# Kernel optimization log

Hardware: AMD Instinct MI355X
Metric: run time of the kernel (lower is better)

## Reference

```python
import jax, jax.numpy as jnp
import numpy as np

BLOCK_SIZE = 32       # MXFP block size (OCP microscaling spec)
E2M1_MAX = 6.0        # max magnitude representable in FP4 E2M1
E2M1_EMAX = 2.0       # exponent of max binade (4..6)


def quantize_mxfp4(t):
    """Fake-quantize t to MXFP4 (E2M1 elements, E8M0 shared scale) along last dim.

    Matches MXFP_F.extract_mxfp_components + dequant: per block of 32 values a
    power-of-two shared scale 2^(floor(log2(amax)) - emax_elem), elements
    rounded to nearest E2M1 value {0, +-0.5, 1, 1.5, 2, 3, 4, 6}.
    """
    shp = t.shape
    tb = t.reshape(shp[:-1] + (shp[-1] // BLOCK_SIZE, BLOCK_SIZE))
    amax = jnp.max(jnp.abs(tb), axis=-1, keepdims=True)
    safe_amax = jnp.where(amax > 0, amax, 1.0)
    shared_exp = jnp.floor(jnp.log2(safe_amax)) - E2M1_EMAX  # E8M0 exponent
    scale = jnp.exp2(shared_exp)
    v = tb / scale
    av = jnp.abs(v)
    # E2M1 grid spacing: 0.5 in [0,2), 1 in [2,4), 2 in [4,6]
    e = jnp.clip(jnp.floor(jnp.log2(jnp.maximum(av, 2.0 ** -10))), 0.0, E2M1_EMAX)
    step = jnp.exp2(e - 1.0)  # one mantissa bit
    q = jnp.clip(jnp.round(av / step) * step, 0.0, E2M1_MAX) * jnp.sign(v)
    return (q * scale).reshape(shp)


def setup_inputs() -> dict:
    key = jax.random.key(0)
    kx, kw, kb = jax.random.split(key, 3)
    B, S, K, N = 2, 4096, 4096, 4096
    x = jax.random.normal(kx, (B, S, K), dtype=jnp.float32)
    weight = jax.random.normal(kw, (N, K), dtype=jnp.float32) * 0.02
    bias = jax.random.normal(kb, (N,), dtype=jnp.float32) * 0.02
    return {"x": x, "weight": weight, "bias": bias}


def reference(x, weight, bias):
    # layer_type 'XqWqB': quantize activations (block along in_features) and
    # weights (block_dim=1 == in_features); bias stays full precision.
    xq = quantize_mxfp4(x)                 # [B, S, K]
    wq = quantize_mxfp4(weight)            # [N, K]
    out = jnp.einsum("bsk,nk->bsn", xq, wq) + bias
    return out
```

## Files before the change

kernel.cpp:

```cpp
#include <hip/hip_runtime.h>
#include <hip/hip_bf16.h>

typedef __attribute__((ext_vector_type(4))) int i32x4;
typedef __attribute__((ext_vector_type(8))) int i32x8;
typedef __attribute__((ext_vector_type(16))) float f32x16;

#define GLOBAL_CPTR(x) ((__attribute__((address_space(1))) const void*)(x))
#define LDS_PTR(x)     ((__attribute__((address_space(3))) void*)(x))

__global__ __launch_bounds__(256) void mxfp4_quant_pack_kernel(
    const float* __restrict__ xin, unsigned char* __restrict__ xq,
    unsigned char* __restrict__ xsc, const float* __restrict__ win,
    unsigned char* __restrict__ wq, unsigned char* __restrict__ wsc,
    int kshift, int gx) {
  const int KC = 1 << (kshift - 5);
  const int CQ = KC >> 2;
  const int bid0 = blockIdx.x;
  const float* in;
  unsigned char* outq;
  unsigned char* outsc;
  int bid;
  if (bid0 < gx) { in = xin; outq = xq; outsc = xsc; bid = bid0; }
  else           { in = win; outq = wq; outsc = wsc; bid = bid0 - gx; }

  const int cq  = bid & (CQ - 1);
  const int R   = (bid >> (kshift - 7)) << 6;
  const int t   = threadIdx.x;

  __shared__ float sf[64 * 132];

  const float* base = in + ((size_t)R << kshift) + (cq << 7);
#pragma unroll
  for (int i = 0; i < 8; ++i) {
    const int g   = i * 256 + t;
    const int row = g >> 5;
    const int c4  = g & 31;
    float4 v = *reinterpret_cast<const float4*>(
        base + ((size_t)row << kshift) + (c4 << 2));
    *reinterpret_cast<float4*>(sf + row * 132 + (c4 << 2)) = v;
  }
  __syncthreads();

  const int rl = (t & 3) + ((t >> 4) << 2);
  const int kc = (t >> 2) & 3;
  const float* src = sf + rl * 132 + (kc << 5);
  float v[32];
#pragma unroll
  for (int i = 0; i < 8; ++i)
    *reinterpret_cast<float4*>(v + 4 * i) =
        *reinterpret_cast<const float4*>(src + 4 * i);

  float am = 0.f;
#pragma unroll
  for (int j = 0; j < 32; ++j) am = fmaxf(am, fabsf(v[j]));

  const float safe = am > 0.f ? am : 1.f;
  const int se = ilogbf(safe) - 2;
  const float inv = ldexpf(1.f, -se);

  unsigned int packs[4] = {0, 0, 0, 0};
#pragma unroll
  for (int j = 0; j < 32; ++j) {
    const float val = v[j] * inv;
    const float av = fabsf(val);
    const float avc = fmaxf(av, 9.765625e-4f);
    int ee = (int)((__float_as_uint(avc) >> 23) & 0xFF) - 127;
    ee = ee < 0 ? 0 : (ee > 2 ? 2 : ee);
    const float istep = __uint_as_float((unsigned)(128 - ee) << 23);
    const int m = (int)rintf(av * istep);
    unsigned int c = (unsigned)(m + (ee << 1));
    c = c > 7u ? 7u : c;
    c |= (__float_as_uint(val) >> 28) & 8u;
    packs[j >> 3] |= c << (4 * (j & 7));
  }

  const int row = R + rl;
  const size_t chunk = (size_t)(row >> 8) * KC + (cq << 2) + kc;
  *reinterpret_cast<uint4*>(outq + chunk * 4096 + (size_t)(row & 255) * 16) =
      make_uint4(packs[0], packs[1], packs[2], packs[3]);
  outsc[chunk * 256 + (row & 31) * 8 + ((row >> 5) & 7)] =
      (unsigned char)(se + 127);
}

#define BM 256
#define BN 256
#define NTHR 512
#define BUFS 18432

__global__ __launch_bounds__(NTHR, 2) void mxfp_gemm_kernel(
    const unsigned char* __restrict__ Aq, const unsigned char* __restrict__ Asc,
    const unsigned char* __restrict__ Bq, const unsigned char* __restrict__ Bsc,
    const float* __restrict__ bias, float* __restrict__ C,
    int M, int N, int K) {
  __shared__ unsigned char lds[2 * BUFS];

  const int tid = threadIdx.x;
  const int l   = tid & 63;
  const int wid = tid >> 6;
  const int wm  = wid >> 2;
  const int wn  = wid & 3;

  const int nwg = gridDim.x;
  const int bid = blockIdx.x;
  const int swz = (bid & 7) * (nwg >> 3) + (bid >> 3);
  const int nbn = N / BN;
  const int bm  = swz / nbn;
  const int bn  = swz % nbn;

  const int KC = K >> 5;

  const unsigned char* bLane = Bq + (((size_t)bn * KC) << 12) +
                               ((size_t)(l >> 5) << 12) + (wn << 10) +
                               ((l & 31) << 4);

  f32x16 acc[4][2] = {};

#define STAGE(BUFO, KT)                                                        \
  do {                                                                         \
    const int cl = wid & 3;                                                    \
    const int rg2 = (wid >> 2) << 1;                                           \
    const size_t abase = ((size_t)bm * KC + (size_t)(KT) * 4 + cl) * 4096;     \
    _Pragma("unroll") for (int i = 0; i < 2; ++i) {                            \
      __builtin_amdgcn_global_load_lds(                                        \
          GLOBAL_CPTR(Aq + abase + (rg2 + i) * 1024 + (l << 4)),               \
          LDS_PTR(lds + (BUFO) + cl * 4096 + (rg2 + i) * 1024), 16, 0, 0);     \
    }                                                                          \
    if (wid < 4) {                                                             \
      __builtin_amdgcn_global_load_lds(                                        \
          GLOBAL_CPTR(Asc + ((size_t)bm * KC + (size_t)(KT) * 4 + wid) * 256   \
                      + (l << 2)),                                             \
          LDS_PTR(lds + (BUFO) + 16384 + wid * 256), 4, 0, 0);                 \
    } else {                                                                   \
      __builtin_amdgcn_global_load_lds(                                        \
          GLOBAL_CPTR(Bsc + ((size_t)bn * KC + (size_t)(KT) * 4 + (wid - 4))   \
                      * 256 + (l << 2)),                                       \
          LDS_PTR(lds + (BUFO) + 17408 + (wid - 4) * 256), 4, 0, 0);           \
    }                                                                          \
  } while (0)

#define MFMA1(MB, NB, AV, BV)                                                  \
  acc[MB][NB] = __builtin_amdgcn_mfma_scale_f32_32x32x64_f8f6f4(               \
      a8[MB], b8[NB], acc[MB][NB], 4, 4, MB, AV, NB, BV)

#define KTILE(BUFO, KT)                                                        \
  do {                                                                         \
    const i32x4 z4 = {0, 0, 0, 0};                                             \
    const unsigned char* bt = bLane + ((size_t)(KT) << 14);                    \
    i32x4 braw[2][2];                                                          \
    _Pragma("unroll") for (int ks = 0; ks < 2; ++ks)                           \
      _Pragma("unroll") for (int nb = 0; nb < 2; ++nb)                         \
        braw[ks][nb] =                                                         \
            *(const i32x4*)(bt + (ks << 13) + (nb << 9));                      \
    _Pragma("unroll") for (int ks = 0; ks < 2; ++ks) {                         \
      const int cofs = (ks << 13) + ((l & 32) << 7);    \
      i32x8 a8[4], b8[2];                                                      \
      _Pragma("unroll") for (int mb = 0; mb < 4; ++mb)                         \
        a8[mb] = __builtin_shufflevector(                                      \
            *(const i32x4*)(lds + (BUFO) + cofs +                              \
                            (((wm << 7) + (mb << 5) + (l & 31)) << 4)),        \
            z4, 0, 1, 2, 3, 4, 5, 6, 7);                                       \
      _Pragma("unroll") for (int nb = 0; nb < 2; ++nb)                         \
        b8[nb] = __builtin_shufflevector(braw[ks][nb], z4,                     \
                                         0, 1, 2, 3, 4, 5, 6, 7);              \
      const int av = *(const int*)(lds + (BUFO) + 16384 + (cofs >> 4) +        \
                                   ((l & 31) << 3) + (wm << 2));               \
      const int bv = *(const ushort*)(lds + (BUFO) + 17408 + (cofs >> 4) +     \
                                      ((l & 31) << 3) + (wn << 1));            \
      MFMA1(0, 0, av, bv); MFMA1(0, 1, av, bv);                                \
      MFMA1(1, 0, av, bv); MFMA1(1, 1, av, bv);                                \
      MFMA1(2, 0, av, bv); MFMA1(2, 1, av, bv);                                \
      MFMA1(3, 0, av, bv); MFMA1(3, 1, av, bv);                                \
    }                                                                          \
  } while (0)

  STAGE(0, 0);
  asm volatile("s_waitcnt vmcnt(0)" ::: "memory");
  __builtin_amdgcn_s_barrier();
  asm volatile("" ::: "memory");

  const int NKT = K >> 7;
  for (int t = 0; t < NKT; ++t) {
    const int tn = (t + 1 < NKT) ? (t + 1) : t;
    const int bufC = (t & 1) ? BUFS : 0;
    const int bufN = (t & 1) ? 0 : BUFS;
    STAGE(bufN, tn);
    KTILE(bufC, t);
    asm volatile("s_waitcnt vmcnt(0)" ::: "memory");
    __builtin_amdgcn_s_barrier();
    asm volatile("" ::: "memory");
  }

  const int colb = bn * BN + wn * 64 + (l & 31);
  const int rowb = bm * BM + wm * 128 + ((l >> 5) << 2);
  const float bv0 = bias[colb];
  const float bv1 = bias[colb + 32];
#pragma unroll
  for (int mb = 0; mb < 4; ++mb) {
#pragma unroll
    for (int nb = 0; nb < 2; ++nb) {
      const float bv = nb ? bv1 : bv0;
      const int col = colb + nb * 32;
#pragma unroll
      for (int r = 0; r < 16; ++r) {
        const int row = rowb + mb * 32 + ((r >> 2) << 3) + (r & 3);
        C[(size_t)row * N + col] = acc[mb][nb][r] + bv;
      }
    }
  }
}

extern "C" void kernel_launch(void* const* d_in, const int* in_sizes, int n_in,
                              void* d_out, int out_size, void* d_ws, size_t ws_size,
                              hipStream_t stream) {
  const float* x    = (const float*)d_in[0];
  const float* w    = (const float*)d_in[1];
  const float* bias = (const float*)d_in[2];
  float* out = (float*)d_out;

  const int N = in_sizes[2];
  const int K = in_sizes[1] / N;
  const int M = (int)((long long)in_sizes[0] / K);
  const int kshift = __builtin_ctz(K);

  unsigned char* xq  = (unsigned char*)d_ws;
  unsigned char* wq  = xq + ((size_t)M * K >> 1);
  unsigned char* xsc = wq + ((size_t)N * K >> 1);
  unsigned char* wsc = xsc + ((size_t)M * K >> 5);

  const int CQ = (K >> 5) >> 2;
  const int gx = (M >> 6) * CQ;
  const int gw = (N >> 6) * CQ;

  mxfp4_quant_pack_kernel<<<dim3((unsigned)(gx + gw)), dim3(256), 0, stream>>>(
      x, xq, xsc, w, wq, wsc, kshift, gx);

  dim3 grid((M / BM) * (N / BN));
  mxfp_gemm_kernel<<<grid, dim3(NTHR), 0, stream>>>(xq, xsc, wq, wsc, bias, out,
                                                    M, N, K);
}
```

Before: 147.4 us.

## Shrink GEMM tile to 128x256 with 4 waves and stage B through LDS

The GEMM block tile drops from 256x256 with 8 waves to 128x256 with 4 waves. B tiles and scales are now staged through LDS with async global-to-LDS loads, where before each wave read them directly from global memory into registers. The A-side addressing and scale indexing are remapped onto the half-tile of the 256-row packed layout. The intent is more blocks and waves per CU (launch bounds raised to 3) and B fetches that overlap through the double buffer, at the cost of half the A reuse per block and more LDS per buffer.

```diff
diff --git a/kernel.cpp b/kernel.cpp
--- a/kernel.cpp
+++ b/kernel.cpp
@@ -82,12 +82,12 @@
       (unsigned char)(se + 127);
 }
 
-#define BM 256
+#define BM 128
 #define BN 256
-#define NTHR 512
-#define BUFS 18432
-
-__global__ __launch_bounds__(NTHR, 2) void mxfp_gemm_kernel(
+#define NTHR 256
+#define BUFS 26624
+
+__global__ __launch_bounds__(NTHR, 3) void mxfp_gemm_kernel(
     const unsigned char* __restrict__ Aq, const unsigned char* __restrict__ Asc,
     const unsigned char* __restrict__ Bq, const unsigned char* __restrict__ Bsc,
     const float* __restrict__ bias, float* __restrict__ C,
@@ -97,8 +97,7 @@
   const int tid = threadIdx.x;
   const int l   = tid & 63;
   const int wid = tid >> 6;
-  const int wm  = wid >> 2;
-  const int wn  = wid & 3;
+  const int wn  = wid;
 
   const int nwg = gridDim.x;
   const int bid = blockIdx.x;
@@ -109,62 +108,56 @@
 
   const int KC = K >> 5;
 
-  const unsigned char* bLane = Bq + (((size_t)bn * KC) << 12) +
-                               ((size_t)(l >> 5) << 12) + (wn << 10) +
-                               ((l & 31) << 4);
-
   f32x16 acc[4][2] = {};
 
 #define STAGE(BUFO, KT)                                                        \
   do {                                                                         \
-    const int cl = wid & 3;                                                    \
-    const int rg2 = (wid >> 2) << 1;                                           \
-    const size_t abase = ((size_t)bm * KC + (size_t)(KT) * 4 + cl) * 4096;     \
-    _Pragma("unroll") for (int i = 0; i < 2; ++i) {                            \
+    const size_t t4 = (size_t)(KT) * 4;                                        \
+    const size_t abase =                                                       \
+        ((size_t)(bm >> 1) * KC + t4 + wid) * 4096 + ((bm & 1) << 11);         \
+    _Pragma("unroll") for (int h = 0; h < 2; ++h)                              \
       __builtin_amdgcn_global_load_lds(                                        \
-          GLOBAL_CPTR(Aq + abase + (rg2 + i) * 1024 + (l << 4)),               \
-          LDS_PTR(lds + (BUFO) + cl * 4096 + (rg2 + i) * 1024), 16, 0, 0);     \
-    }                                                                          \
-    if (wid < 4) {                                                             \
+          GLOBAL_CPTR(Aq + abase + h * 1024 + (l << 4)),                       \
+          LDS_PTR(lds + (BUFO) + wid * 2048 + h * 1024), 16, 0, 0);            \
+    _Pragma("unroll") for (int c = 0; c < 4; ++c)                              \
       __builtin_amdgcn_global_load_lds(                                        \
-          GLOBAL_CPTR(Asc + ((size_t)bm * KC + (size_t)(KT) * 4 + wid) * 256   \
-                      + (l << 2)),                                             \
-          LDS_PTR(lds + (BUFO) + 16384 + wid * 256), 4, 0, 0);                 \
-    } else {                                                                   \
-      __builtin_amdgcn_global_load_lds(                                        \
-          GLOBAL_CPTR(Bsc + ((size_t)bn * KC + (size_t)(KT) * 4 + (wid - 4))   \
-                      * 256 + (l << 2)),                                       \
-          LDS_PTR(lds + (BUFO) + 17408 + (wid - 4) * 256), 4, 0, 0);           \
-    }                                                                          \
+          GLOBAL_CPTR(Bq + ((size_t)bn * KC + t4 + c) * 4096 + (wid << 10) +   \
+                      (l << 4)),                                               \
+          LDS_PTR(lds + (BUFO) + 8192 + c * 4096 + (wid << 10)), 16, 0, 0);    \
+    __builtin_amdgcn_global_load_lds(                                          \
+        GLOBAL_CPTR(Asc + ((size_t)(bm >> 1) * KC + t4 + wid) * 256 +          \
+                    (l << 2)),                                                 \
+        LDS_PTR(lds + (BUFO) + 24576 + (wid << 8)), 4, 0, 0);                  \
+    __builtin_amdgcn_global_load_lds(                                          \
+        GLOBAL_CPTR(Bsc + ((size_t)bn * KC + t4 + wid) * 256 + (l << 2)),      \
+        LDS_PTR(lds + (BUFO) + 25600 + (wid << 8)), 4, 0, 0);                  \
   } while (0)
 
 #define MFMA1(MB, NB, AV, BV)                                                  \
   acc[MB][NB] = __builtin_amdgcn_mfma_scale_f32_32x32x64_f8f6f4(               \
       a8[MB], b8[NB], acc[MB][NB], 4, 4, MB, AV, NB, BV)
 
-#define KTILE(BUFO, KT)                                                        \
+#define KTILE(BUFO)                                                            \
   do {                                                                         \
     const i32x4 z4 = {0, 0, 0, 0};                                             \
-    const unsigned char* bt = bLane + ((size_t)(KT) << 14);                    \
-    i32x4 braw[2][2];                                                          \
-    _Pragma("unroll") for (int ks = 0; ks < 2; ++ks)                           \
-      _Pragma("unroll") for (int nb = 0; nb < 2; ++nb)                         \
-        braw[ks][nb] =                                                         \
-            *(const i32x4*)(bt + (ks << 13) + (nb << 9));                      \
     _Pragma("unroll") for (int ks = 0; ks < 2; ++ks) {                         \
-      const int cofs = (ks << 13) + ((l & 32) << 7);    \
+      const int cofsA = (ks << 12) + ((l & 32) << 6);          \
+      const int cofsB = (ks << 13) + ((l & 32) << 7);          \
+      const int scofs = (ks << 9) + ((l & 32) << 3);           \
       i32x8 a8[4], b8[2];                                                      \
       _Pragma("unroll") for (int mb = 0; mb < 4; ++mb)                         \
         a8[mb] = __builtin_shufflevector(                                      \
-            *(const i32x4*)(lds + (BUFO) + cofs +                              \
-                            (((wm << 7) + (mb << 5) + (l & 31)) << 4)),        \
+            *(const i32x4*)(lds + (BUFO) + cofsA +                             \
+                            (((mb << 5) + (l & 31)) << 4)),                    \
             z4, 0, 1, 2, 3, 4, 5, 6, 7);                                       \
       _Pragma("unroll") for (int nb = 0; nb < 2; ++nb)                         \
-        b8[nb] = __builtin_shufflevector(braw[ks][nb], z4,                     \
-                                         0, 1, 2, 3, 4, 5, 6, 7);              \
-      const int av = *(const int*)(lds + (BUFO) + 16384 + (cofs >> 4) +        \
-                                   ((l & 31) << 3) + (wm << 2));               \
-      const int bv = *(const ushort*)(lds + (BUFO) + 17408 + (cofs >> 4) +     \
+        b8[nb] = __builtin_shufflevector(                                      \
+            *(const i32x4*)(lds + (BUFO) + 8192 + cofsB +                      \
+                            (((wn << 6) + (nb << 5) + (l & 31)) << 4)),        \
+            z4, 0, 1, 2, 3, 4, 5, 6, 7);                                       \
+      const int av = *(const int*)(lds + (BUFO) + 24576 + scofs +              \
+                                   ((l & 31) << 3) + ((bm & 1) << 2));         \
+      const int bv = *(const ushort*)(lds + (BUFO) + 25600 + scofs +           \
                                       ((l & 31) << 3) + (wn << 1));            \
       MFMA1(0, 0, av, bv); MFMA1(0, 1, av, bv);                                \
       MFMA1(1, 0, av, bv); MFMA1(1, 1, av, bv);                                \
@@ -184,14 +177,14 @@
     const int bufC = (t & 1) ? BUFS : 0;
     const int bufN = (t & 1) ? 0 : BUFS;
     STAGE(bufN, tn);
-    KTILE(bufC, t);
+    KTILE(bufC);
     asm volatile("s_waitcnt vmcnt(0)" ::: "memory");
     __builtin_amdgcn_s_barrier();
     asm volatile("" ::: "memory");
   }
 
   const int colb = bn * BN + wn * 64 + (l & 31);
-  const int rowb = bm * BM + wm * 128 + ((l >> 5) << 2);
+  const int rowb = bm * BM + ((l >> 5) << 2);
   const float bv0 = bias[colb];
   const float bv1 = bias[colb + 32];
 #pragma unroll
```

Result: faster. 135.1 us, median of 2 (-8.3%).
